# Optimization experiments

Measured on AMD Instinct MI355X. Metric: run time of the kernel, lower is better.

Reference implementation:

```python
import jax, jax.numpy as jnp
import numpy as np

H, D = 16, 64            # heads_num, mouse_hidden_dim // heads_num
START_FRAME = 9728       # current_start (token units)
GLOBAL_END_PREV = 9728   # kv_cache['global_end_index'] before this call
LOCAL_END_PREV = 9728    # kv_cache['local_end_index'] before this call
SINK = 0                 # sink_tokens in source
WINDOW = 8192            # max_attention_size = local_attn_size (token units)


def _rope_interleaved(x, cos_h, sin_h):
    # non-neox (interleaved) rotary: x [B,S,H,D], cos_h/sin_h [S, D//2]
    x1 = x[..., 0::2]
    x2 = x[..., 1::2]
    c = cos_h[None, :, None, :]
    s = sin_h[None, :, None, :]
    o1 = x1 * c - x2 * s
    o2 = x2 * c + x1 * s
    return jnp.stack([o1, o2], axis=-1).reshape(x.shape)


def setup_inputs() -> dict:
    key = jax.random.key(0)
    ks = jax.random.split(key, 7)
    B, S, C = 1, 1024, 10240
    return {
        'q': jax.random.normal(ks[0], (B, S, H, D), jnp.float32),
        'k': jax.random.normal(ks[1], (B, S, H, D), jnp.float32),
        'v': jax.random.normal(ks[2], (B, S, H, D), jnp.float32),
        'cache_k': jax.random.normal(ks[3], (B, C, H, D), jnp.float32),
        'cache_v': jax.random.normal(ks[4], (B, C, H, D), jnp.float32),
        'freqs_cos': jax.random.uniform(ks[5], (START_FRAME + S, D), jnp.float32, -1.0, 1.0),
        'freqs_sin': jax.random.uniform(ks[6], (START_FRAME + S, D), jnp.float32, -1.0, 1.0),
    }


def reference(q, k, v, cache_k, cache_v, freqs_cos, freqs_sin):
    B, S, _, _ = q.shape
    # _apply_rotary_emb_qk: slice freqs at start_offset, take every-other col (cos_half)
    cos_h = freqs_cos[START_FRAME:START_FRAME + S, ::2]  # [S, D//2]
    sin_h = freqs_sin[START_FRAME:START_FRAME + S, ::2]
    q_r = _rope_interleaved(q, cos_h, sin_h)
    k_r = _rope_interleaved(k, cos_h, sin_h)

    # ring-buffer KV-cache update (all index math is static Python ints)
    current_end = START_FRAME + S
    cache_size = cache_k.shape[1]
    num_new = S
    if current_end > GLOBAL_END_PREV and num_new + LOCAL_END_PREV > cache_size:
        num_evicted = num_new + LOCAL_END_PREV - cache_size
        num_rolled = LOCAL_END_PREV - num_evicted - SINK
        rolled_k = jax.lax.dynamic_slice_in_dim(cache_k, SINK + num_evicted, num_rolled, axis=1)
        rolled_v = jax.lax.dynamic_slice_in_dim(cache_v, SINK + num_evicted, num_rolled, axis=1)
        cache_k = cache_k.at[:, SINK:SINK + num_rolled].set(rolled_k)
        cache_v = cache_v.at[:, SINK:SINK + num_rolled].set(rolled_v)
        local_end = LOCAL_END_PREV + current_end - GLOBAL_END_PREV - num_evicted
    else:
        local_end = LOCAL_END_PREV + current_end - GLOBAL_END_PREV
    local_start = local_end - num_new
    cache_k = cache_k.at[:, local_start:local_end].set(k_r)
    cache_v = cache_v.at[:, local_start:local_end].set(v)

    # windowed (last local_attn_size tokens) non-causal attention
    cache_start = max(0, local_end - WINDOW)
    wk = cache_k[:, cache_start:local_end]  # [B, W, H, D]
    wv = cache_v[:, cache_start:local_end]
    scale = 1.0 / np.float32(np.sqrt(D))
    scores = jnp.einsum('bqhd,bkhd->bhqk', q_r, wk) * scale
    probs = jax.nn.softmax(scores, axis=-1)
    out = jnp.einsum('bhqk,bkhd->bqhd', probs, wv)
    return out.reshape(B, S, H * D)
```

## Files before the change

### kernel.cpp

```cpp
#include <hip/hip_runtime.h>

#define HH 16
#define DD 64
#define SQ 1024
#define LW 8192
#define OLDK 7168
#define CACHE_BASE 2560
#define SFRAME 9728
#define KSPLIT 8
#define KPER (LW / KSPLIT)
#define NSTEP (KPER / 64)

#define KB_OFF 0u
#define VT_OFF 16777216u
#define QB_OFF 33554432u
#define OP_OFF 35651584u
#define LP_OFF 69206016u

typedef __bf16 bf16x8 __attribute__((ext_vector_type(8)));
typedef float floatx16 __attribute__((ext_vector_type(16)));
typedef unsigned uintx2 __attribute__((ext_vector_type(2)));
typedef unsigned uintx4 __attribute__((ext_vector_type(4)));

__device__ __forceinline__ unsigned short f2bf(float f) {
  unsigned u = __builtin_bit_cast(unsigned, f);
  u += 0x7fffu + ((u >> 16) & 1u);
  return (unsigned short)(u >> 16);
}

__device__ __forceinline__ float fast_exp2(float x) {
#if __has_builtin(__builtin_amdgcn_exp2f)
  return __builtin_amdgcn_exp2f(x);
#else
  return __builtin_exp2f(x);
#endif
}

__device__ __forceinline__ unsigned pack_bf2(float a, float b) {
#if __has_builtin(__builtin_amdgcn_cvt_pk_bf16_f32)
  typedef __bf16 bf16x2_t __attribute__((ext_vector_type(2)));
  bf16x2_t r = __builtin_amdgcn_cvt_pk_bf16_f32(a, b);
  return __builtin_bit_cast(unsigned, r);
#else
  unsigned ua = __builtin_bit_cast(unsigned, a) + 0x8000u;
  unsigned ub = __builtin_bit_cast(unsigned, b) + 0x8000u;
  return __builtin_amdgcn_perm(ub, ua, 0x07060302);
#endif
}

__device__ __forceinline__ void async16(void* lds, const void* g) {
  __builtin_amdgcn_global_load_lds((__attribute__((address_space(1))) void*)(g),
                                   (__attribute__((address_space(3))) void*)(lds),
                                   16, 0, 0);
}

__global__ __launch_bounds__(256) void prepass(
    const float* __restrict__ qin, const float* __restrict__ kin,
    const float* __restrict__ vin, const float* __restrict__ ck,
    const float* __restrict__ cv, const float* __restrict__ fc,
    const float* __restrict__ fs, unsigned short* __restrict__ Kb,
    unsigned short* __restrict__ Vt, unsigned short* __restrict__ Qb) {
  int b = blockIdx.x, t = threadIdx.x;
  if (b < 2048) {
    __shared__ float tl[64 * 65];
    int h = b >> 7, kk0 = (b & 127) * 64;
    int col = t & 63, rb = t >> 6;
#pragma unroll
    for (int i = 0; i < 16; i++) {
      int r = i * 4 + rb;
      int kk = kk0 + r;
      float val = (kk < OLDK) ? cv[(CACHE_BASE + kk) * (HH * DD) + h * DD + col]
                              : vin[(kk - OLDK) * (HH * DD) + h * DD + col];
      tl[r * 65 + col] = val;
    }
    __syncthreads();
#pragma unroll
    for (int i = 0; i < 16; i++) {
      int d = i * 4 + rb;
      Vt[(h * DD + d) * LW + kk0 + col] = f2bf(tl[col * 65 + d]);
    }
  } else if (b < 9216) {
    int b1 = b - 2048;
    int h = b1 / 448, g = b1 % 448;
    int kk = g * 16 + (t >> 4);
    int lane = t & 15;
    float4 val = *(const float4*)(ck + (CACHE_BASE + kk) * (HH * DD) + h * DD + lane * 4);
    ushort4 o;
    o.x = f2bf(val.x); o.y = f2bf(val.y); o.z = f2bf(val.z); o.w = f2bf(val.w);
    *(ushort4*)(Kb + (h * LW + kk) * DD + lane * 4) = o;
  } else if (b < 11264) {
    int b2 = b - 9216;
    int rh = b2 * 8 + (t >> 5);
    int s = rh >> 4, h = rh & 15, i = t & 31;
    float2 x = *(const float2*)(kin + s * (HH * DD) + h * DD + 2 * i);
    float c = fc[(SFRAME + s) * DD + 2 * i];
    float sn = fs[(SFRAME + s) * DD + 2 * i];
    ushort2 o;
    o.x = f2bf(x.x * c - x.y * sn);
    o.y = f2bf(x.y * c + x.x * sn);
    *(ushort2*)(Kb + (h * LW + OLDK + s) * DD + 2 * i) = o;
  } else {
    int b3 = b - 11264;
    int rh = b3 * 8 + (t >> 5);
    int s = rh >> 4, h = rh & 15, i = t & 31;
    const float SC = 0.18033688011112042f;
    float2 x = *(const float2*)(qin + s * (HH * DD) + h * DD + 2 * i);
    float c = fc[(SFRAME + s) * DD + 2 * i];
    float sn = fs[(SFRAME + s) * DD + 2 * i];
    ushort2 o;
    o.x = f2bf((x.x * c - x.y * sn) * SC);
    o.y = f2bf((x.y * c + x.x * sn) * SC);
    *(ushort2*)(Qb + (h * SQ + s) * DD + 2 * i) = o;
  }
}

__global__ __launch_bounds__(256, 2) void attn(
    const unsigned short* __restrict__ Kb, const unsigned short* __restrict__ Vt,
    const unsigned short* __restrict__ Qb, float* __restrict__ Op,
    float* __restrict__ Lp) {
  __shared__ __align__(16) unsigned char sK[8192];
  __shared__ __align__(16) unsigned char sV[8192];

  int bid = blockIdx.x;
  int g = bid & 127, qb = bid >> 7;
  int h = g & 15, ks = g >> 4;
  int t = threadIdx.x;
  int w = t >> 6, lane = t & 63;
  int l31 = lane & 31, e = lane >> 5;
  int sw = l31 & 7;
  int q0 = qb * 256 + w * 64;

  bf16x8 qf[2][4];
#pragma unroll
  for (int tq = 0; tq < 2; tq++) {
    const unsigned short* qptr = Qb + (h * SQ + q0 + 32 * tq + l31) * DD + 8 * e;
#pragma unroll
    for (int c = 0; c < 4; c++) qf[tq][c] = *(const bf16x8*)(qptr + 16 * c);
  }

  floatx16 o[2][2];
#pragma unroll
  for (int a = 0; a < 2; a++)
#pragma unroll
    for (int bb = 0; bb < 2; bb++)
#pragma unroll
      for (int i = 0; i < 16; i++) o[a][bb][i] = 0.f;
  float ls[2] = {0.f, 0.f};

  const unsigned short* KbH = Kb + h * (LW * DD);
  const unsigned short* VtH = Vt + h * (DD * LW);
  int kkBase = ks * KPER;

  for (int st = 0; st < NSTEP; st++) {
    int kk0 = kkBase + st * 64;
    __syncthreads();
#pragma unroll
    for (int hf = 0; hf < 2; hf++) {
      int gi = w * 128 + hf * 64 + lane;
      int rr = gi >> 3;
      int bs = (gi & 7) ^ (rr & 7);
      async16(sK + gi * 16, KbH + (kk0 + rr) * DD + bs * 8);
      async16(sV + gi * 16, VtH + rr * LW + kk0 + bs * 8);
    }
    __syncthreads();

    floatx16 s[2][2];
#pragma unroll
    for (int a = 0; a < 2; a++)
#pragma unroll
      for (int bb = 0; bb < 2; bb++)
#pragma unroll
        for (int i = 0; i < 16; i++) s[a][bb][i] = 0.f;
#pragma unroll
    for (int c = 0; c < 4; c++) {
      int gsl = (2 * c + e) ^ sw;
      bf16x8 ka = *(const bf16x8*)(sK + (l31 * 8 + gsl) * 16);
      bf16x8 kb = *(const bf16x8*)(sK + ((l31 + 32) * 8 + gsl) * 16);
      s[0][0] = __builtin_amdgcn_mfma_f32_32x32x16_bf16(ka, qf[0][c], s[0][0], 0, 0, 0);
      s[0][1] = __builtin_amdgcn_mfma_f32_32x32x16_bf16(kb, qf[0][c], s[0][1], 0, 0, 0);
      s[1][0] = __builtin_amdgcn_mfma_f32_32x32x16_bf16(ka, qf[1][c], s[1][0], 0, 0, 0);
      s[1][1] = __builtin_amdgcn_mfma_f32_32x32x16_bf16(kb, qf[1][c], s[1][1], 0, 0, 0);
    }

    unsigned pk[2][2][4][2];
#pragma unroll
    for (int tq = 0; tq < 2; tq++) {
#pragma unroll
      for (int tk = 0; tk < 2; tk++) {
#pragma unroll
        for (int i = 0; i < 16; i++) s[tq][tk][i] = fast_exp2(s[tq][tk][i]);
        float ps = 0.f;
#pragma unroll
        for (int i = 0; i < 16; i++) ps += s[tq][tk][i];
        ls[tq] += ps;
#pragma unroll
        for (int b = 0; b < 4; b++)
#pragma unroll
          for (int p = 0; p < 2; p++)
            pk[tq][tk][b][p] = pack_bf2(s[tq][tk][4 * b + 2 * p], s[tq][tk][4 * b + 2 * p + 1]);
      }
    }

    bf16x8 pf[2][4];
#pragma unroll
    for (int tq = 0; tq < 2; tq++) {
#pragma unroll
      for (int tk = 0; tk < 2; tk++) {
#pragma unroll
        for (int kcp = 0; kcp < 2; kcp++) {
          uintx2 r0 = __builtin_amdgcn_permlane32_swap(pk[tq][tk][2 * kcp][0],
                                                       pk[tq][tk][2 * kcp + 1][0], false, false);
          uintx2 r1 = __builtin_amdgcn_permlane32_swap(pk[tq][tk][2 * kcp][1],
                                                       pk[tq][tk][2 * kcp + 1][1], false, false);
          uintx4 f;
          f[0] = r0[0]; f[1] = r1[0]; f[2] = r0[1]; f[3] = r1[1];
          pf[tq][2 * tk + kcp] = __builtin_bit_cast(bf16x8, f);
        }
      }
    }

#pragma unroll
    for (int kc = 0; kc < 4; kc++) {
      int gsl = (2 * kc + e) ^ sw;
      bf16x8 va = *(const bf16x8*)(sV + (l31 * 8 + gsl) * 16);
      bf16x8 vb = *(const bf16x8*)(sV + ((l31 + 32) * 8 + gsl) * 16);
      o[0][0] = __builtin_amdgcn_mfma_f32_32x32x16_bf16(va, pf[0][kc], o[0][0], 0, 0, 0);
      o[0][1] = __builtin_amdgcn_mfma_f32_32x32x16_bf16(vb, pf[0][kc], o[0][1], 0, 0, 0);
      o[1][0] = __builtin_amdgcn_mfma_f32_32x32x16_bf16(va, pf[1][kc], o[1][0], 0, 0, 0);
      o[1][1] = __builtin_amdgcn_mfma_f32_32x32x16_bf16(vb, pf[1][kc], o[1][1], 0, 0, 0);
    }
  }

#pragma unroll
  for (int tq = 0; tq < 2; tq++) {
    float l = ls[tq];
    l += __shfl_xor(l, 32, 64);
    int qrow = q0 + 32 * tq + l31;
    float* op = Op + (((ks * 16 + h) * SQ) + qrow) * DD;
#pragma unroll
    for (int t4 = 0; t4 < 4; t4++) {
      float4 a, b;
      a.x = o[tq][0][4 * t4 + 0]; a.y = o[tq][0][4 * t4 + 1];
      a.z = o[tq][0][4 * t4 + 2]; a.w = o[tq][0][4 * t4 + 3];
      b.x = o[tq][1][4 * t4 + 0]; b.y = o[tq][1][4 * t4 + 1];
      b.z = o[tq][1][4 * t4 + 2]; b.w = o[tq][1][4 * t4 + 3];
      *(float4*)(op + 8 * t4 + 4 * e) = a;
      *(float4*)(op + 32 + 8 * t4 + 4 * e) = b;
    }
    if (e == 0) Lp[(ks * 16 + h) * SQ + qrow] = l;
  }
}

__global__ __launch_bounds__(256) void combine(const float* __restrict__ Op,
                                               const float* __restrict__ Lp,
                                               float* __restrict__ out) {
  int idx = blockIdx.x * 256 + threadIdx.x;
  int d = idx & 63, q = (idx >> 6) & 1023, h = idx >> 16;
  float num = 0.f, den = 0.f;
#pragma unroll
  for (int s = 0; s < KSPLIT; s++) {
    int row = (s * 16 + h) * SQ + q;
    num += Op[row * DD + d];
    den += Lp[row];
  }
  out[q * (HH * DD) + h * DD + d] = num / den;
}

extern "C" void kernel_launch(void* const* d_in, const int* in_sizes, int n_in,
                              void* d_out, int out_size, void* d_ws, size_t ws_size,
                              hipStream_t stream) {
  const float* q  = (const float*)d_in[0];
  const float* k  = (const float*)d_in[1];
  const float* v  = (const float*)d_in[2];
  const float* ck = (const float*)d_in[3];
  const float* cv = (const float*)d_in[4];
  const float* fc = (const float*)d_in[5];
  const float* fs = (const float*)d_in[6];
  float* out = (float*)d_out;
  char* ws = (char*)d_ws;

  unsigned short* Kb = (unsigned short*)(ws + KB_OFF);
  unsigned short* Vt = (unsigned short*)(ws + VT_OFF);
  unsigned short* Qb = (unsigned short*)(ws + QB_OFF);
  float* Op = (float*)(ws + OP_OFF);
  float* Lp = (float*)(ws + LP_OFF);

  prepass<<<13312, 256, 0, stream>>>(q, k, v, ck, cv, fc, fs, Kb, Vt, Qb);
  attn<<<512, 256, 0, stream>>>(Kb, Vt, Qb, Op, Lp);
  combine<<<4096, 256, 0, stream>>>(Op, Lp, out);
}
```

Before: 186.6 us.

## Double-buffer K/V tiles in attention and vectorize the V transpose prepass

The attention kernel now keeps two LDS buffers for K and V and issues async loads for the next 64-key tile before computing on the current one, so global-to-LDS latency overlaps with the MFMA work. The XOR swizzle also mixes in the row-group bits so the a/b half-tile reads hit different banks. In the prepass, the V transpose now uses 128-key tiles with float4 loads, an XOR-swizzled LDS layout, and 8-element bf16 stores per thread, which cuts block count and memory transactions. The extra buffers double LDS use per block, which may limit occupancy.

Result: no change. 188.6 us (+1.1%).

```diff
diff --git a/kernel.cpp b/kernel.cpp
--- a/kernel.cpp
+++ b/kernel.cpp
@@ -61,26 +61,42 @@
     const float* __restrict__ fs, unsigned short* __restrict__ Kb,
     unsigned short* __restrict__ Vt, unsigned short* __restrict__ Qb) {
   int b = blockIdx.x, t = threadIdx.x;
-  if (b < 2048) {
-    __shared__ float tl[64 * 65];
-    int h = b >> 7, kk0 = (b & 127) * 64;
-    int col = t & 63, rb = t >> 6;
-#pragma unroll
-    for (int i = 0; i < 16; i++) {
-      int r = i * 4 + rb;
-      int kk = kk0 + r;
-      float val = (kk < OLDK) ? cv[(CACHE_BASE + kk) * (HH * DD) + h * DD + col]
-                              : vin[(kk - OLDK) * (HH * DD) + h * DD + col];
-      tl[r * 65 + col] = val;
+  if (b < 1024) {
+    __shared__ float tl[128 * 64];
+    int h = b >> 6, kk0 = (b & 63) * 128;
+    int c = t & 15;
+#pragma unroll
+    for (int it = 0; it < 8; it++) {
+      int kk = it * 16 + (t >> 4);
+      int gk = kk0 + kk;
+      const float* src = (gk < OLDK)
+                             ? cv + (CACHE_BASE + gk) * (HH * DD) + h * DD + 4 * c
+                             : vin + (gk - OLDK) * (HH * DD) + h * DD + 4 * c;
+      float4 vv = *(const float4*)src;
+      int cg = c ^ (kk >> 3);
+      *(float4*)(tl + kk * 64 + cg * 4) = vv;
     }
     __syncthreads();
-#pragma unroll
-    for (int i = 0; i < 16; i++) {
-      int d = i * 4 + rb;
-      Vt[(h * DD + d) * LW + kk0 + col] = f2bf(tl[col * 65 + d]);
-    }
-  } else if (b < 9216) {
-    int b1 = b - 2048;
+    int kq = t & 15;
+#pragma unroll
+    for (int jt = 0; jt < 4; jt++) {
+      int d = jt * 16 + (t >> 4);
+      ushort4 lo, hi;
+      unsigned short tmp[8];
+#pragma unroll
+      for (int j = 0; j < 8; j++) {
+        int kk = 8 * kq + j;
+        int cg = (d >> 2) ^ kq;
+        tmp[j] = f2bf(tl[kk * 64 + cg * 4 + (d & 3)]);
+      }
+      lo.x = tmp[0]; lo.y = tmp[1]; lo.z = tmp[2]; lo.w = tmp[3];
+      hi.x = tmp[4]; hi.y = tmp[5]; hi.z = tmp[6]; hi.w = tmp[7];
+      unsigned short* dst = Vt + (h * DD + d) * LW + kk0 + 8 * kq;
+      *(ushort4*)(dst) = lo;
+      *(ushort4*)(dst + 4) = hi;
+    }
+  } else if (b < 8192) {
+    int b1 = b - 1024;
     int h = b1 / 448, g = b1 % 448;
     int kk = g * 16 + (t >> 4);
     int lane = t & 15;
@@ -88,8 +104,8 @@
     ushort4 o;
     o.x = f2bf(val.x); o.y = f2bf(val.y); o.z = f2bf(val.z); o.w = f2bf(val.w);
     *(ushort4*)(Kb + (h * LW + kk) * DD + lane * 4) = o;
-  } else if (b < 11264) {
-    int b2 = b - 9216;
+  } else if (b < 10240) {
+    int b2 = b - 8192;
     int rh = b2 * 8 + (t >> 5);
     int s = rh >> 4, h = rh & 15, i = t & 31;
     float2 x = *(const float2*)(kin + s * (HH * DD) + h * DD + 2 * i);
@@ -100,7 +116,7 @@
     o.y = f2bf(x.y * c + x.x * sn);
     *(ushort2*)(Kb + (h * LW + OLDK + s) * DD + 2 * i) = o;
   } else {
-    int b3 = b - 11264;
+    int b3 = b - 10240;
     int rh = b3 * 8 + (t >> 5);
     int s = rh >> 4, h = rh & 15, i = t & 31;
     const float SC = 0.18033688011112042f;
@@ -118,8 +134,8 @@
     const unsigned short* __restrict__ Kb, const unsigned short* __restrict__ Vt,
     const unsigned short* __restrict__ Qb, float* __restrict__ Op,
     float* __restrict__ Lp) {
-  __shared__ __align__(16) unsigned char sK[8192];
-  __shared__ __align__(16) unsigned char sV[8192];
+  __shared__ __align__(16) unsigned char sK[2][8192];
+  __shared__ __align__(16) unsigned char sV[2][8192];
 
   int bid = blockIdx.x;
   int g = bid & 127, qb = bid >> 7;
@@ -127,8 +143,10 @@
   int t = threadIdx.x;
   int w = t >> 6, lane = t & 63;
   int l31 = lane & 31, e = lane >> 5;
-  int sw = l31 & 7;
   int q0 = qb * 256 + w * 64;
+
+  int baseA = (l31 & 7) ^ ((l31 >> 3) & 7);
+  int baseB = (l31 & 7) ^ (((l31 >> 3) + 4) & 7);
 
   bf16x8 qf[2][4];
 #pragma unroll
@@ -151,18 +169,24 @@
   const unsigned short* VtH = Vt + h * (DD * LW);
   int kkBase = ks * KPER;
 
-  for (int st = 0; st < NSTEP; st++) {
-    int kk0 = kkBase + st * 64;
-    __syncthreads();
+  auto stage = [&](int buf, int kk0) {
 #pragma unroll
     for (int hf = 0; hf < 2; hf++) {
       int gi = w * 128 + hf * 64 + lane;
       int rr = gi >> 3;
-      int bs = (gi & 7) ^ (rr & 7);
-      async16(sK + gi * 16, KbH + (kk0 + rr) * DD + bs * 8);
-      async16(sV + gi * 16, VtH + rr * LW + kk0 + bs * 8);
-    }
+      int src = (gi & 7) ^ (rr & 7) ^ ((rr >> 3) & 7);
+      async16(sK[buf] + gi * 16, KbH + (kk0 + rr) * DD + src * 8);
+      async16(sV[buf] + gi * 16, VtH + rr * LW + kk0 + src * 8);
+    }
+  };
+
+  stage(0, kkBase);
+
+  for (int st = 0; st < NSTEP; st++) {
     __syncthreads();
+    if (st + 1 < NSTEP) stage((st + 1) & 1, kkBase + (st + 1) * 64);
+    const unsigned char* cK = sK[st & 1];
+    const unsigned char* cV = sV[st & 1];
 
     floatx16 s[2][2];
 #pragma unroll
@@ -173,9 +197,10 @@
         for (int i = 0; i < 16; i++) s[a][bb][i] = 0.f;
 #pragma unroll
     for (int c = 0; c < 4; c++) {
-      int gsl = (2 * c + e) ^ sw;
-      bf16x8 ka = *(const bf16x8*)(sK + (l31 * 8 + gsl) * 16);
-      bf16x8 kb = *(const bf16x8*)(sK + ((l31 + 32) * 8 + gsl) * 16);
+      int pA = (2 * c + e) ^ baseA;
+      int pB = (2 * c + e) ^ baseB;
+      bf16x8 ka = *(const bf16x8*)(cK + (l31 * 8 + pA) * 16);
+      bf16x8 kb = *(const bf16x8*)(cK + ((l31 + 32) * 8 + pB) * 16);
       s[0][0] = __builtin_amdgcn_mfma_f32_32x32x16_bf16(ka, qf[0][c], s[0][0], 0, 0, 0);
       s[0][1] = __builtin_amdgcn_mfma_f32_32x32x16_bf16(kb, qf[0][c], s[0][1], 0, 0, 0);
       s[1][0] = __builtin_amdgcn_mfma_f32_32x32x16_bf16(ka, qf[1][c], s[1][0], 0, 0, 0);
@@ -194,10 +219,10 @@
         for (int i = 0; i < 16; i++) ps += s[tq][tk][i];
         ls[tq] += ps;
 #pragma unroll
-        for (int b = 0; b < 4; b++)
+        for (int bq = 0; bq < 4; bq++)
 #pragma unroll
           for (int p = 0; p < 2; p++)
-            pk[tq][tk][b][p] = pack_bf2(s[tq][tk][4 * b + 2 * p], s[tq][tk][4 * b + 2 * p + 1]);
+            pk[tq][tk][bq][p] = pack_bf2(s[tq][tk][4 * bq + 2 * p], s[tq][tk][4 * bq + 2 * p + 1]);
       }
     }
 
@@ -221,9 +246,10 @@
 
 #pragma unroll
     for (int kc = 0; kc < 4; kc++) {
-      int gsl = (2 * kc + e) ^ sw;
-      bf16x8 va = *(const bf16x8*)(sV + (l31 * 8 + gsl) * 16);
-      bf16x8 vb = *(const bf16x8*)(sV + ((l31 + 32) * 8 + gsl) * 16);
+      int pA = (2 * kc + e) ^ baseA;
+      int pB = (2 * kc + e) ^ baseB;
+      bf16x8 va = *(const bf16x8*)(cV + (l31 * 8 + pA) * 16);
+      bf16x8 vb = *(const bf16x8*)(cV + ((l31 + 32) * 8 + pB) * 16);
       o[0][0] = __builtin_amdgcn_mfma_f32_32x32x16_bf16(va, pf[0][kc], o[0][0], 0, 0, 0);
       o[0][1] = __builtin_amdgcn_mfma_f32_32x32x16_bf16(vb, pf[0][kc], o[0][1], 0, 0, 0);
       o[1][0] = __builtin_amdgcn_mfma_f32_32x32x16_bf16(va, pf[1][kc], o[1][0], 0, 0, 0);
@@ -285,7 +311,7 @@
   float* Op = (float*)(ws + OP_OFF);
   float* Lp = (float*)(ws + LP_OFF);
 
-  prepass<<<13312, 256, 0, stream>>>(q, k, v, ck, cv, fc, fs, Kb, Vt, Qb);
+  prepass<<<12288, 256, 0, stream>>>(q, k, v, ck, cv, fc, fs, Kb, Vt, Qb);
   attn<<<512, 256, 0, stream>>>(Kb, Vt, Qb, Op, Lp);
   combine<<<4096, 256, 0, stream>>>(Op, Lp, out);
 }
```
